# Kernel optimization log

Hardware: AMD Instinct MI355X
Metric: run time of the kernel (lower is better)

## Reference

```python
import jax, jax.numpy as jnp
import numpy as np

B, T, D = 2, 2048, 1024
NH, NKV, HD = 16, 4, 64
KD = NKV * HD          # 256
PD = 16                # rope partial dim (rotated dims)
RANK = 8
ALPHA = 1.0
ROPE_BASE = 10000.0


def setup_inputs() -> dict:
    key = jax.random.key(0)
    ks = jax.random.split(key, 10)
    s = 0.02
    return {
        "x":      jax.random.normal(ks[0], (B, T, D), jnp.float32),
        "Wq":     jax.random.normal(ks[1], (D, D), jnp.float32) * s,
        "Wk":     jax.random.normal(ks[2], (KD, D), jnp.float32) * s,
        "Wv":     jax.random.normal(ks[3], (KD, D), jnp.float32) * s,
        "Wproj":  jax.random.normal(ks[4], (D, D), jnp.float32) * s,
        "q_gain": jnp.full((NH,), 5.25, jnp.float32),
        "Aq":     jax.random.normal(ks[5], (RANK, D), jnp.float32) * s,
        "Bq":     jax.random.normal(ks[6], (D, RANK), jnp.float32) * s,
        "Av":     jax.random.normal(ks[7], (RANK, D), jnp.float32) * s,
        "Bv":     jax.random.normal(ks[8], (KD, RANK), jnp.float32) * s,
    }


def _rms_norm(x):
    # F.rms_norm with no weight: x / sqrt(mean(x^2) + eps), eps = dtype machine eps
    eps = jnp.finfo(x.dtype).eps
    return x * jax.lax.rsqrt(jnp.mean(x * x, axis=-1, keepdims=True) + eps)


def _rope_partial(x, cos, sin, pd):
    # x: [B, T, H, HD]; rotate first pd dims (half/half), pass rest through
    h = pd // 2
    x1, x2, rest = x[..., :h], x[..., h:pd], x[..., pd:]
    c = cos[None, :, None, :]  # [1, T, 1, h]
    s = sin[None, :, None, :]
    return jnp.concatenate([x1 * c + x2 * s, -x2 * c + x1 * s, rest], axis=-1)


def reference(x, Wq, Wk, Wv, Wproj, q_gain, Aq, Bq, Av, Bv):
    # projections + per-step LoRA on Q and V (output = alpha * B(A(x)))
    q = x @ Wq.T + ALPHA * ((x @ Aq.T) @ Bq.T)          # [B,T,D]
    k = x @ Wk.T                                        # [B,T,KD]
    v = x @ Wv.T + ALPHA * ((x @ Av.T) @ Bv.T)          # [B,T,KD]

    q = _rms_norm(q.reshape(B, T, NH, HD))
    k = _rms_norm(k.reshape(B, T, NKV, HD))
    v = v.reshape(B, T, NKV, HD)

    # partial RoPE tables: [T, PD//2]
    inv = 1.0 / (ROPE_BASE ** (jnp.arange(0, PD, 2, dtype=jnp.float32) / PD))
    freqs = jnp.arange(T, dtype=jnp.float32)[:, None] * inv[None, :]
    cos, sin = jnp.cos(freqs), jnp.sin(freqs)
    q = _rope_partial(q, cos, sin, PD)
    k = _rope_partial(k, cos, sin, PD)

    # learned per-head QK gain on queries
    q = q * q_gain[None, None, :, None]

    # GQA: repeat-interleave kv heads to NH
    g = NH // NKV
    kf = jnp.repeat(k, g, axis=2)  # [B,T,NH,HD]
    vf = jnp.repeat(v, g, axis=2)

    scale = 1.0 / np.float32(np.sqrt(HD))
    scores = jnp.einsum('bqhd,bkhd->bhqk', q, kf) * scale  # [B,NH,T,T]
    causal = jnp.tril(jnp.ones((T, T), bool))
    scores = jnp.where(causal[None, None], scores, -jnp.inf)
    p = jax.nn.softmax(scores, axis=-1)
    y = jnp.einsum('bhqk,bkhd->bqhd', p, vf).reshape(B, T, D)
    return y @ Wproj.T
```

## Files before the change

### kernel.cpp

```cpp
#include <hip/hip_runtime.h>

#define Tn   2048
#define Dn   1024
#define KDn  256
#define NHn  16
#define NKVn 4
#define Rn   4096

typedef short bf16x8 __attribute__((ext_vector_type(8)));
typedef float f32x4  __attribute__((ext_vector_type(4)));
typedef const __attribute__((address_space(1))) unsigned* gas_p;
typedef __attribute__((address_space(3))) unsigned* las_p;

__device__ unsigned short g_q[(size_t)Rn * Dn];
__device__ unsigned short g_k[(size_t)Rn * KDn];
__device__ unsigned short g_vt[(size_t)2 * NKVn * 64 * Tn];
__device__ unsigned short g_y[(size_t)Rn * Dn];
__device__ unsigned short g_xb[(size_t)Rn * Dn];
__device__ unsigned short g_wq[(size_t)Dn * Dn];
__device__ unsigned short g_wk[(size_t)KDn * Dn];
__device__ unsigned short g_wv[(size_t)KDn * Dn];
__device__ unsigned short g_wp[(size_t)Dn * Dn];
__device__ float g_tq[Rn * 8];
__device__ float g_tv[Rn * 8];

static __device__ __forceinline__ float bf2f(unsigned short u) {
    return __uint_as_float(((unsigned)u) << 16);
}
static __device__ __forceinline__ unsigned short f2bf(float f) {
    unsigned u = __float_as_uint(f);
    u += 0x7fffu + ((u >> 16) & 1u);
    return (unsigned short)(u >> 16);
}
static __device__ __forceinline__ unsigned pk2bf(float a, float b) {
    return (unsigned)f2bf(a) | ((unsigned)f2bf(b) << 16);
}
static __device__ __forceinline__ unsigned cvtpk(float a, float b) {
    unsigned r;
    asm("v_cvt_pk_bf16_f32 %0, %1, %2" : "=v"(r) : "v"(a), "v"(b));
    return r;
}
static __device__ __forceinline__ float wave_sum(float s) {
    #pragma unroll
    for (int off = 32; off; off >>= 1) s += __shfl_xor(s, off);
    return s;
}

__global__ __launch_bounds__(256)
void lora_tmp(const float* __restrict__ x,
              const float* __restrict__ Aq,
              const float* __restrict__ Av) {
    int tid = threadIdx.x, wave = tid >> 6, lane = tid & 63;
    int row = blockIdx.x * 4 + wave;
    const float2* xr = (const float2*)(x + (size_t)row * Dn);
    unsigned* xbo = (unsigned*)g_xb + (size_t)row * (Dn / 2);
    float aq[8], av[8];
    #pragma unroll
    for (int r = 0; r < 8; r++) { aq[r] = 0.f; av[r] = 0.f; }
    for (int it = 0; it < Dn / 128; it++) {
        int j = it * 64 + lane;
        float2 xv = xr[j];
        xbo[j] = pk2bf(xv.x, xv.y);
        #pragma unroll
        for (int r = 0; r < 8; r++) {
            float2 a2 = ((const float2*)(Aq + (size_t)r * Dn))[j];
            aq[r] += xv.x * a2.x + xv.y * a2.y;
        }
        #pragma unroll
        for (int r = 0; r < 8; r++) {
            float2 a2 = ((const float2*)(Av + (size_t)r * Dn))[j];
            av[r] += xv.x * a2.x + xv.y * a2.y;
        }
    }
    #pragma unroll
    for (int r = 0; r < 8; r++) { aq[r] = wave_sum(aq[r]); av[r] = wave_sum(av[r]); }
    if (lane == 0) {
        #pragma unroll
        for (int r = 0; r < 8; r++) { g_tq[row * 8 + r] = aq[r]; g_tv[row * 8 + r] = av[r]; }
    }
}

#define NQ4 (Dn * Dn / 4)
#define NK4 (KDn * Dn / 4)
__global__ __launch_bounds__(256)
void cast_w(const float* __restrict__ Wq, const float* __restrict__ Wk,
            const float* __restrict__ Wv, const float* __restrict__ Wp) {
    int i = blockIdx.x * 256 + threadIdx.x;
    const float* src; unsigned short* dst; int o;
    if      (i < NQ4)                 { src = Wq; dst = g_wq; o = i; }
    else if (i < NQ4 + NK4)           { src = Wk; dst = g_wk; o = i - NQ4; }
    else if (i < NQ4 + 2 * NK4)       { src = Wv; dst = g_wv; o = i - NQ4 - NK4; }
    else                              { src = Wp; dst = g_wp; o = i - NQ4 - 2 * NK4; }
    float4 v = ((const float4*)src)[o];
    ((uint2*)dst)[o] = make_uint2(pk2bf(v.x, v.y), pk2bf(v.z, v.w));
}

template<int MODE>
__global__ __launch_bounds__(256, 2)
void gemm_bt(float* __restrict__ Cout, const float* __restrict__ BqL,
             const float* __restrict__ BvL, const float* __restrict__ qgain,
             int M, int K) {
    const unsigned short* A = (MODE == 0) ? g_xb : g_y;

    int gx = gridDim.x;
    int flat = blockIdx.y * gx + blockIdx.x;
    int cpx = (gx * gridDim.y) >> 3;
    int flat2 = (flat & 7) * cpx + (flat >> 3);
    int n0 = (flat2 % gx) * 64, m0 = (flat2 / gx) * 128;

    const unsigned short* W;
    int wroff, region;
    if (MODE == 0) {
        if (n0 < 1024)      { W = g_wq; wroff = n0;        region = 0; }
        else if (n0 < 1280) { W = g_wk; wroff = n0 - 1024; region = 1; }
        else                { W = g_wv; wroff = n0 - 1280; region = 2; }
    } else { W = g_wp; wroff = n0; region = 3; }

    __shared__ __align__(16) unsigned short SM[24576];
    int tid = threadIdx.x;
    int w = tid >> 6, lane = tid & 63;
    int m_ = lane & 15, quad = lane >> 4;

    int lrow = lane >> 3, lseg = (lane & 7) * 8;
    const unsigned short* agp[4];
    #pragma unroll
    for (int i = 0; i < 4; i++)
        agp[i] = A + (size_t)(m0 + w * 32 + i * 8 + lrow) * K + lseg;
    const unsigned short* wgp[2];
    #pragma unroll
    for (int i = 0; i < 2; i++)
        wgp[i] = W + (size_t)(wroff + w * 16 + i * 8 + lrow) * K + lseg;
    int alb[4], wlb[2];
    #pragma unroll
    for (int i = 0; i < 4; i++) alb[i] = (w * 32 + i * 8) * 64;
    #pragma unroll
    for (int i = 0; i < 2; i++) wlb[i] = 16384 + (w * 16 + i * 8) * 64;

    f32x4 acc[2][4];
    #pragma unroll
    for (int im = 0; im < 2; im++)
        #pragma unroll
        for (int in = 0; in < 4; in++) acc[im][in] = (f32x4){0.f, 0.f, 0.f, 0.f};

    #pragma unroll
    for (int i = 0; i < 4; i++)
        __builtin_amdgcn_global_load_lds((gas_p)agp[i], (las_p)&SM[alb[i]], 16, 0, 0);
    #pragma unroll
    for (int i = 0; i < 2; i++)
        __builtin_amdgcn_global_load_lds((gas_p)wgp[i], (las_p)&SM[wlb[i]], 16, 0, 0);

    int nk = K >> 6;
    for (int kt = 0; kt < nk; kt++) {
        __syncthreads();
        int cur = kt & 1, nxt = cur ^ 1;
        if (kt + 1 < nk) {
            int ko = (kt + 1) * 64;
            #pragma unroll
            for (int i = 0; i < 4; i++)
                __builtin_amdgcn_global_load_lds((gas_p)(agp[i] + ko),
                    (las_p)&SM[nxt * 8192 + alb[i]], 16, 0, 0);
            #pragma unroll
            for (int i = 0; i < 2; i++)
                __builtin_amdgcn_global_load_lds((gas_p)(wgp[i] + ko),
                    (las_p)&SM[nxt * 4096 + wlb[i]], 16, 0, 0);
        }
        #pragma unroll
        for (int kk = 0; kk < 2; kk++) {
            bf16x8 bf[4];
            #pragma unroll
            for (int in = 0; in < 4; in++)
                bf[in] = *(const bf16x8*)&SM[16384 + cur * 4096 +
                                             (in * 16 + m_) * 64 + kk * 32 + quad * 8];
            #pragma unroll
            for (int im = 0; im < 2; im++) {
                bf16x8 af = *(const bf16x8*)&SM[cur * 8192 +
                                                (w * 32 + im * 16 + m_) * 64 + kk * 32 + quad * 8];
                #pragma unroll
                for (int in = 0; in < 4; in++)
                    acc[im][in] = __builtin_amdgcn_mfma_f32_16x16x32_bf16(af, bf[in], acc[im][in], 0, 0, 0);
            }
        }
    }

    if (MODE == 1) {
        #pragma unroll
        for (int im = 0; im < 2; im++)
            #pragma unroll
            for (int r = 0; r < 4; r++) {
                int row = m0 + w * 32 + im * 16 + quad * 4 + r;
                #pragma unroll
                for (int in = 0; in < 4; in++)
                    Cout[(size_t)row * Dn + (n0 + in * 16 + m_)] = acc[im][in][r];
            }
        return;
    }

    if (region <= 1) {
        float blc[4][8];
        if (region == 0) {
            #pragma unroll
            for (int in = 0; in < 4; in++) {
                const float* bp = BqL + (size_t)(n0 + in * 16 + m_) * 8;
                #pragma unroll
                for (int j = 0; j < 8; j++) blc[in][j] = bp[j];
            }
        }
        float ghead = (region == 0) ? qgain[n0 >> 6] * 0.18033688011112042f : 1.0f;
        #pragma unroll
        for (int im = 0; im < 2; im++) {
            #pragma unroll
            for (int r = 0; r < 4; r++) {
                int row = m0 + w * 32 + im * 16 + quad * 4 + r;
                float vv[4];
                float ss = 0.f;
                if (region == 0) {
                    const float* tp = g_tq + (size_t)row * 8;
                    float tv8[8];
                    #pragma unroll
                    for (int j = 0; j < 8; j++) tv8[j] = tp[j];
                    #pragma unroll
                    for (int in = 0; in < 4; in++) {
                        float val = acc[im][in][r];
                        #pragma unroll
                        for (int j = 0; j < 8; j++) val += tv8[j] * blc[in][j];
                        vv[in] = val; ss += val * val;
                    }
                } else {
                    #pragma unroll
                    for (int in = 0; in < 4; in++) { vv[in] = acc[im][in][r]; ss += vv[in] * vv[in]; }
                }
                ss += __shfl_xor(ss, 1); ss += __shfl_xor(ss, 2);
                ss += __shfl_xor(ss, 4); ss += __shfl_xor(ss, 8);
                float rs = rsqrtf(ss * (1.0f / 64.0f) + 1.1920929e-7f);
                #pragma unroll
                for (int in = 0; in < 4; in++) vv[in] *= rs;
                float p = __shfl_xor(vv[0], 8);
                int t = row & (Tn - 1);
                float fr = (float)t * exp2f(-(float)(m_ & 7) * 1.6609640474436813f);
                float c = cosf(fr), sn = sinf(fr);
                if (m_ < 16) vv[0] = (m_ < 8) ? vv[0] * c + p * sn : p * sn - vv[0] * c;
                #pragma unroll
                for (int in = 0; in < 4; in++) {
                    float val = vv[in] * ghead;
                    int col = n0 + in * 16 + m_;
                    if (region == 0) g_q[(size_t)row * Dn + col] = f2bf(val);
                    else             g_k[(size_t)row * KDn + (col - 1024)] = f2bf(val);
                }
            }
        }
    } else {
        float blc[4][8];
        #pragma unroll
        for (int in = 0; in < 4; in++) {
            const float* bp = BvL + (size_t)(n0 - 1280 + in * 16 + m_) * 8;
            #pragma unroll
            for (int j = 0; j < 8; j++) blc[in][j] = bp[j];
        }
        __syncthreads();
        #pragma unroll
        for (int im = 0; im < 2; im++) {
            #pragma unroll
            for (int r = 0; r < 4; r++) {
                int rl = w * 32 + im * 16 + quad * 4 + r;
                const float* tp = g_tv + (size_t)(m0 + rl) * 8;
                float tv8[8];
                #pragma unroll
                for (int j = 0; j < 8; j++) tv8[j] = tp[j];
                #pragma unroll
                for (int in = 0; in < 4; in++) {
                    float val = acc[im][in][r];
                    #pragma unroll
                    for (int j = 0; j < 8; j++) val += tv8[j] * blc[in][j];
                    SM[(in * 16 + m_) * 136 + rl] = f2bf(val);
                }
            }
        }
        __syncthreads();
        int d = tid >> 2, tseg = (tid & 3) * 32;
        int bb = m0 >> 11, t0 = m0 & (Tn - 1);
        int kvh = (n0 - 1280) >> 6;
        unsigned short* dst = g_vt + (((size_t)(bb * NKVn + kvh) * 64) + d) * Tn + t0 + tseg;
        const uint4* srcv = (const uint4*)&SM[d * 136 + tseg];
        uint4 c0 = srcv[0], c1 = srcv[1], c2 = srcv[2], c3 = srcv[3];
        ((uint4*)dst)[0] = c0; ((uint4*)dst)[1] = c1;
        ((uint4*)dst)[2] = c2; ((uint4*)dst)[3] = c3;
    }
}

__global__ __launch_bounds__(256, 4)
void attn_kernel() {
    __shared__ __align__(16) unsigned short KS[64 * 72];
    __shared__ __align__(16) unsigned short VS[64 * 72];
    __shared__ __align__(16) unsigned short Pt[4][16 * 72];
    int tid = threadIdx.x;
    int w = tid >> 6, lane = tid & 63;
    int q_ = lane & 15, quad = lane >> 4;
    int b = blockIdx.z, kvh = blockIdx.y, h = kvh * 4 + w;
    int bx = blockIdx.x;
    if ((kvh >> 1) & 1) bx = 127 - bx;
    int qb = bx * 16;
    int qg = qb + q_;

    const unsigned short* qrow =
        g_q + ((size_t)(b * Tn + qg) * NHn + h) * 64 + quad * 8;
    bf16x8 Qf0 = *(const bf16x8*)qrow;
    bf16x8 Qf1 = *(const bf16x8*)(qrow + 32);

    int srow = tid >> 2, sseg = (tid & 3) * 16;
    const unsigned short* kgp =
        g_k + ((size_t)(b * Tn + srow) * NKVn + kvh) * 64 + sseg;
    const unsigned short* vgp =
        g_vt + ((size_t)(b * NKVn + kvh) * 64 + srow) * Tn + sseg;

    f32x4 accO[4];
    #pragma unroll
    for (int i = 0; i < 4; i++) accO[i] = (f32x4){0.f, 0.f, 0.f, 0.f};
    float lsum = 0.f;
    int ntiles = (qb + 79) >> 6;

    {
        uint4 ka = *(const uint4*)kgp, kb = *(const uint4*)(kgp + 8);
        uint4 va = *(const uint4*)vgp, vb = *(const uint4*)(vgp + 8);
        *(uint4*)&KS[srow * 72 + sseg] = ka;
        *(uint4*)&KS[srow * 72 + sseg + 8] = kb;
        *(uint4*)&VS[srow * 72 + sseg] = va;
        *(uint4*)&VS[srow * 72 + sseg + 8] = vb;
    }
    __syncthreads();

    for (int kt = 0; kt < ntiles; kt++) {
        bool pre = (kt + 1 < ntiles);
        uint4 kan, kbn, van, vbn;
        if (pre) {
            const unsigned short* kp = kgp + (size_t)(kt + 1) * (64 * NKVn * 64);
            const unsigned short* vp = vgp + (kt + 1) * 64;
            kan = *(const uint4*)kp; kbn = *(const uint4*)(kp + 8);
            van = *(const uint4*)vp; vbn = *(const uint4*)(vp + 8);
        }

        f32x4 s[4];
        __builtin_amdgcn_s_setprio(1);
        #pragma unroll
        for (int ss = 0; ss < 4; ss++) {
            bf16x8 ka = *(const bf16x8*)&KS[(ss * 16 + q_) * 72 + quad * 8];
            bf16x8 kb = *(const bf16x8*)&KS[(ss * 16 + q_) * 72 + 32 + quad * 8];
            s[ss] = (f32x4){0.f, 0.f, 0.f, 0.f};
            s[ss] = __builtin_amdgcn_mfma_f32_16x16x32_bf16(ka, Qf0, s[ss], 0, 0, 0);
            s[ss] = __builtin_amdgcn_mfma_f32_16x16x32_bf16(kb, Qf1, s[ss], 0, 0, 0);
        }
        __builtin_amdgcn_s_setprio(0);

        if (kt == ntiles - 1) {
            #pragma unroll
            for (int ss = 0; ss < 4; ss++) {
                int k0 = kt * 64 + ss * 16 + quad * 4;
                #pragma unroll
                for (int r = 0; r < 4; r++)
                    if (k0 + r > qg) s[ss][r] = -1e30f;
            }
        }
        float p[4][4];
        #pragma unroll
        for (int ss = 0; ss < 4; ss++)
            #pragma unroll
            for (int r = 0; r < 4; r++) {
                p[ss][r] = exp2f(s[ss][r]);
                lsum += p[ss][r];
            }

        unsigned short* pb = &Pt[w][0];
        #pragma unroll
        for (int ss = 0; ss < 4; ss++)
            *(uint2*)&pb[q_ * 72 + ss * 16 + quad * 4] =
                make_uint2(cvtpk(p[ss][0], p[ss][1]), cvtpk(p[ss][2], p[ss][3]));
        bf16x8 pf0 = *(const bf16x8*)&pb[q_ * 72 + quad * 8];
        bf16x8 pf1 = *(const bf16x8*)&pb[q_ * 72 + 32 + quad * 8];

        __builtin_amdgcn_s_setprio(1);
        #pragma unroll
        for (int c = 0; c < 4; c++) {
            bf16x8 vf0 = *(const bf16x8*)&VS[(c * 16 + q_) * 72 + quad * 8];
            bf16x8 vf1 = *(const bf16x8*)&VS[(c * 16 + q_) * 72 + 32 + quad * 8];
            accO[c] = __builtin_amdgcn_mfma_f32_16x16x32_bf16(vf0, pf0, accO[c], 0, 0, 0);
            accO[c] = __builtin_amdgcn_mfma_f32_16x16x32_bf16(vf1, pf1, accO[c], 0, 0, 0);
        }
        __builtin_amdgcn_s_setprio(0);

        __syncthreads();
        if (pre) {
            *(uint4*)&KS[srow * 72 + sseg] = kan;
            *(uint4*)&KS[srow * 72 + sseg + 8] = kbn;
            *(uint4*)&VS[srow * 72 + sseg] = van;
            *(uint4*)&VS[srow * 72 + sseg + 8] = vbn;
        }
        __syncthreads();
    }

    lsum += __shfl_xor(lsum, 16);
    lsum += __shfl_xor(lsum, 32);
    float invl = 1.0f / lsum;
    unsigned short* yp = g_y + ((size_t)(b * Tn + qg) * NHn + h) * 64;
    #pragma unroll
    for (int c = 0; c < 4; c++) {
        uint2 o = make_uint2(cvtpk(accO[c][0] * invl, accO[c][1] * invl),
                             cvtpk(accO[c][2] * invl, accO[c][3] * invl));
        *(uint2*)&yp[c * 16 + quad * 4] = o;
    }
}

extern "C" void kernel_launch(void* const* d_in, const int* in_sizes, int n_in,
                              void* d_out, int out_size, void* d_ws, size_t ws_size,
                              hipStream_t stream) {
    const float* x  = (const float*)d_in[0];
    const float* Wq = (const float*)d_in[1];
    const float* Wk = (const float*)d_in[2];
    const float* Wv = (const float*)d_in[3];
    const float* Wp = (const float*)d_in[4];
    const float* qg = (const float*)d_in[5];
    const float* Aq = (const float*)d_in[6];
    const float* Bq = (const float*)d_in[7];
    const float* Av = (const float*)d_in[8];
    const float* Bv = (const float*)d_in[9];
    float* out = (float*)d_out;

    lora_tmp<<<dim3(Rn / 4), dim3(256), 0, stream>>>(x, Aq, Av);
    cast_w<<<dim3((NQ4 * 2 + NK4 * 2) / 256), dim3(256), 0, stream>>>(Wq, Wk, Wv, Wp);
    gemm_bt<0><<<dim3(1536 / 64, Rn / 128), dim3(256), 0, stream>>>(
        nullptr, Bq, Bv, qg, Rn, Dn);
    attn_kernel<<<dim3(Tn / 16, NKVn, 2), dim3(256), 0, stream>>>();
    gemm_bt<1><<<dim3(Dn / 64, Rn / 128), dim3(256), 0, stream>>>(
        out, nullptr, nullptr, nullptr, Rn, Dn);
}
```

Baseline: 195.6 us.

## Pair mirrored causal query blocks per attention workgroup to balance work and reuse KV

Each attention workgroup now handles two 16-row query blocks, bx and its mirror 127-bx, so every block does the same total causal work. The K/V tiles staged in shared memory are reused by both blocks, which halves the number of tile loads and barriers per query row. The grid is halved and launch bounds drop to 2 waves per SIMD to leave room for the doubled accumulators and scores. The cost is more registers and fewer resident workgroups, which reduces latency hiding. The old kvh-based block reversal is removed.

```diff
diff --git a/kernel.cpp b/kernel.cpp
--- a/kernel.cpp
+++ b/kernel.cpp
@@ -287,24 +287,27 @@
     }
 }
 
-__global__ __launch_bounds__(256, 4)
+__global__ __launch_bounds__(256, 2)
 void attn_kernel() {
     __shared__ __align__(16) unsigned short KS[64 * 72];
     __shared__ __align__(16) unsigned short VS[64 * 72];
-    __shared__ __align__(16) unsigned short Pt[4][16 * 72];
+    __shared__ __align__(16) unsigned short Pt[4][2][16 * 72];
     int tid = threadIdx.x;
     int w = tid >> 6, lane = tid & 63;
     int q_ = lane & 15, quad = lane >> 4;
     int b = blockIdx.z, kvh = blockIdx.y, h = kvh * 4 + w;
     int bx = blockIdx.x;
-    if ((kvh >> 1) & 1) bx = 127 - bx;
-    int qb = bx * 16;
-    int qg = qb + q_;
-
-    const unsigned short* qrow =
-        g_q + ((size_t)(b * Tn + qg) * NHn + h) * 64 + quad * 8;
-    bf16x8 Qf0 = *(const bf16x8*)qrow;
-    bf16x8 Qf1 = *(const bf16x8*)(qrow + 32);
+    int qbA = bx * 16, qbB = (127 - bx) * 16;
+    int qgA = qbA + q_, qgB = qbB + q_;
+
+    const unsigned short* qrowA =
+        g_q + ((size_t)(b * Tn + qgA) * NHn + h) * 64 + quad * 8;
+    bf16x8 QA0 = *(const bf16x8*)qrowA;
+    bf16x8 QA1 = *(const bf16x8*)(qrowA + 32);
+    const unsigned short* qrowB =
+        g_q + ((size_t)(b * Tn + qgB) * NHn + h) * 64 + quad * 8;
+    bf16x8 QB0 = *(const bf16x8*)qrowB;
+    bf16x8 QB1 = *(const bf16x8*)(qrowB + 32);
 
     int srow = tid >> 2, sseg = (tid & 3) * 16;
     const unsigned short* kgp =
@@ -312,11 +315,15 @@
     const unsigned short* vgp =
         g_vt + ((size_t)(b * NKVn + kvh) * 64 + srow) * Tn + sseg;
 
-    f32x4 accO[4];
-    #pragma unroll
-    for (int i = 0; i < 4; i++) accO[i] = (f32x4){0.f, 0.f, 0.f, 0.f};
-    float lsum = 0.f;
-    int ntiles = (qb + 79) >> 6;
+    f32x4 accA[4], accB[4];
+    #pragma unroll
+    for (int i = 0; i < 4; i++) {
+        accA[i] = (f32x4){0.f, 0.f, 0.f, 0.f};
+        accB[i] = (f32x4){0.f, 0.f, 0.f, 0.f};
+    }
+    float lsumA = 0.f, lsumB = 0.f;
+    int ntA = (qbA + 79) >> 6;
+    int ntB = (qbB + 79) >> 6;
 
     {
         uint4 ka = *(const uint4*)kgp, kb = *(const uint4*)(kgp + 8);
@@ -328,8 +335,9 @@
     }
     __syncthreads();
 
-    for (int kt = 0; kt < ntiles; kt++) {
-        bool pre = (kt + 1 < ntiles);
+    for (int kt = 0; kt < ntB; kt++) {
+        bool pre = (kt + 1 < ntB);
+        bool doA = (kt < ntA);
         uint4 kan, kbn, van, vbn;
         if (pre) {
             const unsigned short* kp = kgp + (size_t)(kt + 1) * (64 * NKVn * 64);
@@ -338,51 +346,90 @@
             van = *(const uint4*)vp; vbn = *(const uint4*)(vp + 8);
         }
 
-        f32x4 s[4];
+        f32x4 sA[4], sB[4];
         __builtin_amdgcn_s_setprio(1);
         #pragma unroll
         for (int ss = 0; ss < 4; ss++) {
             bf16x8 ka = *(const bf16x8*)&KS[(ss * 16 + q_) * 72 + quad * 8];
             bf16x8 kb = *(const bf16x8*)&KS[(ss * 16 + q_) * 72 + 32 + quad * 8];
-            s[ss] = (f32x4){0.f, 0.f, 0.f, 0.f};
-            s[ss] = __builtin_amdgcn_mfma_f32_16x16x32_bf16(ka, Qf0, s[ss], 0, 0, 0);
-            s[ss] = __builtin_amdgcn_mfma_f32_16x16x32_bf16(kb, Qf1, s[ss], 0, 0, 0);
+            sB[ss] = (f32x4){0.f, 0.f, 0.f, 0.f};
+            sB[ss] = __builtin_amdgcn_mfma_f32_16x16x32_bf16(ka, QB0, sB[ss], 0, 0, 0);
+            sB[ss] = __builtin_amdgcn_mfma_f32_16x16x32_bf16(kb, QB1, sB[ss], 0, 0, 0);
+            if (doA) {
+                sA[ss] = (f32x4){0.f, 0.f, 0.f, 0.f};
+                sA[ss] = __builtin_amdgcn_mfma_f32_16x16x32_bf16(ka, QA0, sA[ss], 0, 0, 0);
+                sA[ss] = __builtin_amdgcn_mfma_f32_16x16x32_bf16(kb, QA1, sA[ss], 0, 0, 0);
+            }
         }
         __builtin_amdgcn_s_setprio(0);
 
-        if (kt == ntiles - 1) {
+        if (kt == ntA - 1) {
             #pragma unroll
             for (int ss = 0; ss < 4; ss++) {
                 int k0 = kt * 64 + ss * 16 + quad * 4;
                 #pragma unroll
                 for (int r = 0; r < 4; r++)
-                    if (k0 + r > qg) s[ss][r] = -1e30f;
-            }
-        }
-        float p[4][4];
-        #pragma unroll
-        for (int ss = 0; ss < 4; ss++)
-            #pragma unroll
-            for (int r = 0; r < 4; r++) {
-                p[ss][r] = exp2f(s[ss][r]);
-                lsum += p[ss][r];
-            }
-
-        unsigned short* pb = &Pt[w][0];
-        #pragma unroll
-        for (int ss = 0; ss < 4; ss++)
-            *(uint2*)&pb[q_ * 72 + ss * 16 + quad * 4] =
-                make_uint2(cvtpk(p[ss][0], p[ss][1]), cvtpk(p[ss][2], p[ss][3]));
-        bf16x8 pf0 = *(const bf16x8*)&pb[q_ * 72 + quad * 8];
-        bf16x8 pf1 = *(const bf16x8*)&pb[q_ * 72 + 32 + quad * 8];
+                    if (k0 + r > qgA) sA[ss][r] = -1e30f;
+            }
+        }
+        if (kt == ntB - 1) {
+            #pragma unroll
+            for (int ss = 0; ss < 4; ss++) {
+                int k0 = kt * 64 + ss * 16 + quad * 4;
+                #pragma unroll
+                for (int r = 0; r < 4; r++)
+                    if (k0 + r > qgB) sB[ss][r] = -1e30f;
+            }
+        }
+
+        bf16x8 pA0, pA1;
+        if (doA) {
+            float p[4][4];
+            #pragma unroll
+            for (int ss = 0; ss < 4; ss++)
+                #pragma unroll
+                for (int r = 0; r < 4; r++) {
+                    p[ss][r] = exp2f(sA[ss][r]);
+                    lsumA += p[ss][r];
+                }
+            unsigned short* pb = &Pt[w][0][0];
+            #pragma unroll
+            for (int ss = 0; ss < 4; ss++)
+                *(uint2*)&pb[q_ * 72 + ss * 16 + quad * 4] =
+                    make_uint2(cvtpk(p[ss][0], p[ss][1]), cvtpk(p[ss][2], p[ss][3]));
+            pA0 = *(const bf16x8*)&pb[q_ * 72 + quad * 8];
+            pA1 = *(const bf16x8*)&pb[q_ * 72 + 32 + quad * 8];
+        }
+        bf16x8 pB0, pB1;
+        {
+            float p[4][4];
+            #pragma unroll
+            for (int ss = 0; ss < 4; ss++)
+                #pragma unroll
+                for (int r = 0; r < 4; r++) {
+                    p[ss][r] = exp2f(sB[ss][r]);
+                    lsumB += p[ss][r];
+                }
+            unsigned short* pb = &Pt[w][1][0];
+            #pragma unroll
+            for (int ss = 0; ss < 4; ss++)
+                *(uint2*)&pb[q_ * 72 + ss * 16 + quad * 4] =
+                    make_uint2(cvtpk(p[ss][0], p[ss][1]), cvtpk(p[ss][2], p[ss][3]));
+            pB0 = *(const bf16x8*)&pb[q_ * 72 + quad * 8];
+            pB1 = *(const bf16x8*)&pb[q_ * 72 + 32 + quad * 8];
+        }
 
         __builtin_amdgcn_s_setprio(1);
         #pragma unroll
         for (int c = 0; c < 4; c++) {
             bf16x8 vf0 = *(const bf16x8*)&VS[(c * 16 + q_) * 72 + quad * 8];
             bf16x8 vf1 = *(const bf16x8*)&VS[(c * 16 + q_) * 72 + 32 + quad * 8];
-            accO[c] = __builtin_amdgcn_mfma_f32_16x16x32_bf16(vf0, pf0, accO[c], 0, 0, 0);
-            accO[c] = __builtin_amdgcn_mfma_f32_16x16x32_bf16(vf1, pf1, accO[c], 0, 0, 0);
+            accB[c] = __builtin_amdgcn_mfma_f32_16x16x32_bf16(vf0, pB0, accB[c], 0, 0, 0);
+            accB[c] = __builtin_amdgcn_mfma_f32_16x16x32_bf16(vf1, pB1, accB[c], 0, 0, 0);
+            if (doA) {
+                accA[c] = __builtin_amdgcn_mfma_f32_16x16x32_bf16(vf0, pA0, accA[c], 0, 0, 0);
+                accA[c] = __builtin_amdgcn_mfma_f32_16x16x32_bf16(vf1, pA1, accA[c], 0, 0, 0);
+            }
         }
         __builtin_amdgcn_s_setprio(0);
 
@@ -396,15 +443,21 @@
         __syncthreads();
     }
 
-    lsum += __shfl_xor(lsum, 16);
-    lsum += __shfl_xor(lsum, 32);
-    float invl = 1.0f / lsum;
-    unsigned short* yp = g_y + ((size_t)(b * Tn + qg) * NHn + h) * 64;
+    lsumA += __shfl_xor(lsumA, 16);
+    lsumA += __shfl_xor(lsumA, 32);
+    lsumB += __shfl_xor(lsumB, 16);
+    lsumB += __shfl_xor(lsumB, 32);
+    float invA = 1.0f / lsumA, invB = 1.0f / lsumB;
+    unsigned short* ypA = g_y + ((size_t)(b * Tn + qgA) * NHn + h) * 64;
+    unsigned short* ypB = g_y + ((size_t)(b * Tn + qgB) * NHn + h) * 64;
     #pragma unroll
     for (int c = 0; c < 4; c++) {
-        uint2 o = make_uint2(cvtpk(accO[c][0] * invl, accO[c][1] * invl),
-                             cvtpk(accO[c][2] * invl, accO[c][3] * invl));
-        *(uint2*)&yp[c * 16 + quad * 4] = o;
+        uint2 oA = make_uint2(cvtpk(accA[c][0] * invA, accA[c][1] * invA),
+                              cvtpk(accA[c][2] * invA, accA[c][3] * invA));
+        *(uint2*)&ypA[c * 16 + quad * 4] = oA;
+        uint2 oB = make_uint2(cvtpk(accB[c][0] * invB, accB[c][1] * invB),
+                              cvtpk(accB[c][2] * invB, accB[c][3] * invB));
+        *(uint2*)&ypB[c * 16 + quad * 4] = oB;
     }
 }
 
@@ -427,7 +480,7 @@
     cast_w<<<dim3((NQ4 * 2 + NK4 * 2) / 256), dim3(256), 0, stream>>>(Wq, Wk, Wv, Wp);
     gemm_bt<0><<<dim3(1536 / 64, Rn / 128), dim3(256), 0, stream>>>(
         nullptr, Bq, Bv, qg, Rn, Dn);
-    attn_kernel<<<dim3(Tn / 16, NKVn, 2), dim3(256), 0, stream>>>();
+    attn_kernel<<<dim3(Tn / 32, NKVn, 2), dim3(256), 0, stream>>>();
     gemm_bt<1><<<dim3(Dn / 64, Rn / 128), dim3(256), 0, stream>>>(
         out, nullptr, nullptr, nullptr, Rn, Dn);
 }
```

Measured after the change: 198.2 us. About the same (+1.3%).
